# Kernel optimization log

Measured on AMD Instinct MI355X. Metric: run time of the kernel, lower is better.

## Reference

```python
import jax, jax.numpy as jnp
import numpy as np

VOCAB = 780
HIDDEN = 256
DEPTH = 6
N_NODES = 65536
N_MESS = 131072
MAX_NEI = 5
N_TREES = 2048


def setup_inputs() -> dict:
    key = jax.random.key(0)
    ks = jax.random.split(key, 16)
    s = 0.05  # weight scale to avoid gate saturation
    return {
        "fnode": jax.random.randint(ks[0], (N_NODES,), 0, VOCAB),
        "fmess": jax.random.randint(ks[1], (N_MESS,), 0, N_NODES),
        "node_graph": jax.random.randint(ks[2], (N_NODES, MAX_NEI), 0, N_MESS),
        "mess_graph": jax.random.randint(ks[3], (N_MESS, MAX_NEI), 0, N_MESS),
        "scope_ids": jnp.sort(jax.random.randint(ks[4], (N_NODES,), 0, N_TREES)),
        "emb": jax.random.normal(ks[5], (VOCAB, HIDDEN), jnp.float32) * s,
        "Wz_w": jax.random.normal(ks[6], (2 * HIDDEN, HIDDEN), jnp.float32) * s,
        "Wz_b": jax.random.normal(ks[7], (HIDDEN,), jnp.float32) * s,
        "Wr_w": jax.random.normal(ks[8], (HIDDEN, HIDDEN), jnp.float32) * s,
        "Ur_w": jax.random.normal(ks[9], (HIDDEN, HIDDEN), jnp.float32) * s,
        "Ur_b": jax.random.normal(ks[10], (HIDDEN,), jnp.float32) * s,
        "Wh_w": jax.random.normal(ks[11], (2 * HIDDEN, HIDDEN), jnp.float32) * s,
        "Wh_b": jax.random.normal(ks[12], (HIDDEN,), jnp.float32) * s,
        "out_w": jax.random.normal(ks[13], (2 * HIDDEN, HIDDEN), jnp.float32) * s,
        "out_b": jax.random.normal(ks[14], (HIDDEN,), jnp.float32) * s,
    }


def reference(fnode, fmess, node_graph, mess_graph, scope_ids,
              emb, Wz_w, Wz_b, Wr_w, Ur_w, Ur_b, Wh_w, Wh_b, out_w, out_b):
    x_node = emb[fnode]            # [N, H] embedding lookup
    x = x_node[fmess]              # [M, H] source-node feature per message
    M = mess_graph.shape[0]
    mask = jnp.ones((M, 1), x.dtype).at[0].set(0.0)  # message 0 is padding
    r1 = x @ Wr_w                  # W_r(x), constant across depth (no bias)

    def gru_step(h, _):
        h_nei = h[mess_graph]                                  # [M, K, H] gather
        sum_h = h_nei.sum(axis=1)                              # [M, H]
        z = jax.nn.sigmoid(jnp.concatenate([x, sum_h], 1) @ Wz_w + Wz_b)
        r = jax.nn.sigmoid(r1[:, None, :] + h_nei @ Ur_w + Ur_b)  # [M, K, H]
        sum_gh = (r * h_nei).sum(axis=1)
        pre_h = jnp.tanh(jnp.concatenate([x, sum_gh], 1) @ Wh_w + Wh_b)
        h_new = ((1.0 - z) * sum_h + z * pre_h) * mask
        return h_new, None

    h0 = jnp.zeros((M, HIDDEN), x.dtype)
    h, _ = jax.lax.scan(gru_step, h0, None, length=DEPTH)

    mess_nei = h[node_graph].sum(axis=1)                       # [N, H]
    node_vec = jax.nn.relu(jnp.concatenate([x_node, mess_nei], 1) @ out_w + out_b)

    # per-tree mean over contiguous scopes (segment mean)
    sums = jax.ops.segment_sum(node_vec, scope_ids, num_segments=N_TREES)
    counts = jax.ops.segment_sum(jnp.ones((node_vec.shape[0],), node_vec.dtype),
                                 scope_ids, num_segments=N_TREES)
    return sums / jnp.maximum(counts, 1.0)[:, None]
```

## Files before the change

kernel.cpp:

```cpp
#include <hip/hip_runtime.h>


#define HD 256
#define NNODES 65536
#define NMESS 131072
#define NVOCAB 780
#define NTREES 2048
#define MAXNEI 5
#define BMF 32
#define LDF 264
#define ROWB 768

typedef short bfrag __attribute__((ext_vector_type(8)));
typedef short s16x8 __attribute__((ext_vector_type(8)));
typedef float f32x4v __attribute__((ext_vector_type(4)));
typedef float f32x2 __attribute__((ext_vector_type(2)));
typedef unsigned int u32x4 __attribute__((ext_vector_type(4)));
typedef unsigned int u32x2 __attribute__((ext_vector_type(2)));
typedef unsigned short ush;
typedef unsigned char u8;

__device__ __forceinline__ float bf2f(ush u) {
    union { unsigned int u; float f; } v; v.u = ((unsigned int)u) << 16; return v.f;
}
__device__ __forceinline__ float bfu_lo(unsigned int w) {
    union { unsigned int u; float f; } v; v.u = w << 16; return v.f;
}
__device__ __forceinline__ float bfu_hi(unsigned int w) {
    union { unsigned int u; float f; } v; v.u = w & 0xffff0000u; return v.f;
}
__device__ __forceinline__ ush f2bf_fast(float f) {
    union { float f; unsigned int u; } v; v.f = f;
    return (ush)((v.u + 0x8000u) >> 16);
}
__device__ __forceinline__ unsigned int pack2bf(float hi, float lo) {
    union { float f; unsigned int u; } a, b; a.f = hi; b.f = lo;
    return __builtin_amdgcn_perm(a.u + 0x8000u, b.u + 0x8000u, 0x07060302u);
}
__device__ __forceinline__ float sigm(float x) {
    return __builtin_amdgcn_rcpf(1.f + __expf(-x));
}
__device__ __forceinline__ float tanh_fast(float x) {
    return 1.f - 2.f * __builtin_amdgcn_rcpf(__expf(2.f * x) + 1.f);
}
__device__ __forceinline__ u32x2 pack8fp8(const float* f) {
    int lo = __builtin_amdgcn_cvt_pk_fp8_f32(f[0], f[1], 0, 0);
    lo = __builtin_amdgcn_cvt_pk_fp8_f32(f[2], f[3], lo, 1);
    int hi = __builtin_amdgcn_cvt_pk_fp8_f32(f[4], f[5], 0, 0);
    hi = __builtin_amdgcn_cvt_pk_fp8_f32(f[6], f[7], hi, 1);
    u32x2 o; o.x = (unsigned int)lo; o.y = (unsigned int)hi; return o;
}
__device__ __forceinline__ void fp8x8_to_f32(u32x2 v, float* f) {
    f32x2 a = __builtin_amdgcn_cvt_pk_f32_fp8((int)v.x, false);
    f32x2 b = __builtin_amdgcn_cvt_pk_f32_fp8((int)v.x, true);
    f32x2 c = __builtin_amdgcn_cvt_pk_f32_fp8((int)v.y, false);
    f32x2 d = __builtin_amdgcn_cvt_pk_f32_fp8((int)v.y, true);
    f[0] = a.x; f[1] = a.y; f[2] = b.x; f[3] = b.y;
    f[4] = c.x; f[5] = c.y; f[6] = d.x; f[7] = d.y;
}

__global__ __launch_bounds__(256) void prep_tables_sk(
    const float* __restrict__ emb,
    const float* __restrict__ Wz_w, const float* __restrict__ Wz_b,
    const float* __restrict__ Wr_w, const float* __restrict__ Ur_b,
    const float* __restrict__ Wh_w, const float* __restrict__ Wh_b,
    const float* __restrict__ out_w, const float* __restrict__ out_b,
    float* __restrict__ embR, float* __restrict__ embZ,
    float* __restrict__ embH, float* __restrict__ embO)
{
    __shared__ __align__(16) float e[4][64];
    int t = threadIdx.x;
    int b0 = blockIdx.x * 4;
    int k0 = blockIdx.y * 64;
    e[t >> 6][t & 63] = emb[(b0 + (t >> 6)) * HD + k0 + (t & 63)];
    __syncthreads();
    float aR[4] = {0,0,0,0}, aZ[4] = {0,0,0,0}, aH[4] = {0,0,0,0}, aO[4] = {0,0,0,0};
    for (int kk = 0; kk < 64; kk++) {
        int k = k0 + kk;
        float wr = Wr_w[k * HD + t];
        float wz = Wz_w[k * HD + t];
        float wh = Wh_w[k * HD + t];
        float wo = out_w[k * HD + t];
        #pragma unroll
        for (int r = 0; r < 4; r++) {
            float ev = e[r][kk];
            aR[r] += ev * wr; aZ[r] += ev * wz; aH[r] += ev * wh; aO[r] += ev * wo;
        }
    }
    if (blockIdx.y == 0) {
        float br = Ur_b[t], bz = Wz_b[t], bh = Wh_b[t], bo = out_b[t];
        #pragma unroll
        for (int r = 0; r < 4; r++) { aR[r] += br; aZ[r] += bz; aH[r] += bh; aO[r] += bo; }
    }
    #pragma unroll
    for (int r = 0; r < 4; r++) {
        atomicAdd(&embR[(b0 + r) * HD + t], aR[r]);
        atomicAdd(&embZ[(b0 + r) * HD + t], aZ[r]);
        atomicAdd(&embH[(b0 + r) * HD + t], aH[r]);
        atomicAdd(&embO[(b0 + r) * HD + t], aO[r]);
    }
}

__global__ __launch_bounds__(256) void h1fill(
    const float* __restrict__ embZ, const float* __restrict__ embH,
    ush* __restrict__ h1tab)
{
    int i = blockIdx.x * HD + threadIdx.x;
    h1tab[i] = f2bf_fast(sigm(embZ[i]) * tanh_fast(embH[i]));
}

__global__ __launch_bounds__(256) void h1u_sk(
    const ush* __restrict__ h1tab, const float* __restrict__ Ur_w,
    float* __restrict__ embU)
{
    __shared__ __align__(16) float e[4][64];
    int t = threadIdx.x;
    int b0 = blockIdx.x * 4;
    int k0 = blockIdx.y * 64;
    e[t >> 6][t & 63] = bf2f(h1tab[(b0 + (t >> 6)) * HD + k0 + (t & 63)]);
    __syncthreads();
    float aU[4] = {0,0,0,0};
    for (int kk = 0; kk < 64; kk++) {
        float w = Ur_w[(k0 + kk) * HD + t];
        #pragma unroll
        for (int r = 0; r < 4; r++) aU[r] += e[r][kk] * w;
    }
    #pragma unroll
    for (int r = 0; r < 4; r++) atomicAdd(&embU[(b0 + r) * HD + t], aU[r]);
}

__global__ __launch_bounds__(256) void prep_wt(
    const float* __restrict__ Ur_w, const float* __restrict__ Wz_w,
    const float* __restrict__ Wh_w, const float* __restrict__ out_w,
    ush* __restrict__ Wo_p,
    ush* __restrict__ Wz_p, ush* __restrict__ Wh_p, ush* __restrict__ Ur_p)
{
    int idx = blockIdx.x * 256 + threadIdx.x;
    int n = idx >> 8, k = idx & 255;
    int paddr = ((((n >> 4) * 8 + (k >> 5)) * 64 + ((k >> 3) & 3) * 16 + (n & 15)) << 3) + (k & 7);
    Wo_p[paddr] = f2bf_fast(out_w[(HD + k) * HD + n]);
    Wz_p[paddr] = f2bf_fast(Wz_w[(HD + k) * HD + n]);
    Wh_p[paddr] = f2bf_fast(Wh_w[(HD + k) * HD + n]);
    Ur_p[paddr] = f2bf_fast(Ur_w[k * HD + n]);
}

__global__ __launch_bounds__(256) void prep_vmess(
    const int* __restrict__ fnode, const int* __restrict__ fmess,
    int* __restrict__ v_mess)
{
    int m = blockIdx.x * 256 + threadIdx.x;
    v_mess[m] = fnode[fmess[m]];
}

__global__ __launch_bounds__(256) void fill_h1(
    const ush* __restrict__ h1tab, const float* __restrict__ embU,
    const int* __restrict__ v_mess, u8* __restrict__ HM)
{
    int t = blockIdx.x * 256 + threadIdx.x;
    int m = t >> 5;
    int c = (t & 31) * 8;
    int v = v_mess[m];
    s16x8 o = *(const s16x8*)&h1tab[v * HD + c];
    float u[8];
    *(float4*)&u[0] = *(const float4*)&embU[v * HD + c];
    *(float4*)&u[4] = *(const float4*)&embU[v * HD + c + 4];
    u32x2 up = pack8fp8(u);
    if (m == 0) { o = (s16x8){0,0,0,0,0,0,0,0}; up.x = up.y = 0; }
    u8* row = HM + (size_t)m * ROWB;
    *(s16x8*)(row + 2 * c) = o;
    *(u32x2*)(row + 512 + c) = up;
}

template<int EMIT_HU>
__global__ __launch_bounds__(256, 4) void fused_step(
    const u8* __restrict__ HM, const int* __restrict__ mg,
    const int* __restrict__ v_mess,
    const float* __restrict__ embR, const float* __restrict__ embZ,
    const float* __restrict__ embH,
    const ush* __restrict__ Wz_p, const ush* __restrict__ Wh_p,
    const ush* __restrict__ Ur_p,
    u8* __restrict__ HM_next)
{
    __shared__ __align__(16) ush sh[BMF * LDF];
    __shared__ __align__(16) ush sg[BMF * LDF];
    int tid = threadIdx.x;
    int wv = tid >> 6, lane = tid & 63;
    int quad = lane >> 4, l16 = lane & 15;
    int m0 = blockIdx.x * BMF;

    #pragma unroll 2
    for (int it = 0; it < 4; it++) {
        int g = it * 256 + tid;
        int ml = g >> 5;
        int c = (g & 31) * 8;
        int m = m0 + ml;
        int v = v_mess[m];
        float rb[8];
        *(float4*)&rb[0] = *(const float4*)&embR[v * HD + c];
        *(float4*)&rb[4] = *(const float4*)&embR[v * HD + c + 4];
        float ah[8] = {0,0,0,0,0,0,0,0};
        float ag[8] = {0,0,0,0,0,0,0,0};
        #pragma unroll
        for (int kn = 0; kn < MAXNEI; kn++) {
            int j = mg[m * MAXNEI + kn];
            const u8* row = HM + (size_t)j * ROWB;
            s16x8 hv = *(const s16x8*)(row + 2 * c);
            u32x2 uv8 = *(const u32x2*)(row + 512 + c);
            float uf[8];
            fp8x8_to_f32(uv8, uf);
            #pragma unroll
            for (int e = 0; e < 8; e++) {
                float hf = bf2f((ush)hv[e]);
                ah[e] += hf;
                ag[e] += sigm(rb[e] + uf[e]) * hf;
            }
        }
        uint4 oh, og;
        oh.x = pack2bf(ah[1], ah[0]); oh.y = pack2bf(ah[3], ah[2]);
        oh.z = pack2bf(ah[5], ah[4]); oh.w = pack2bf(ah[7], ah[6]);
        og.x = pack2bf(ag[1], ag[0]); og.y = pack2bf(ag[3], ag[2]);
        og.z = pack2bf(ag[5], ag[4]); og.w = pack2bf(ag[7], ag[6]);
        *(uint4*)&sh[ml * LDF + c] = oh;
        *(uint4*)&sg[ml * LDF + c] = og;
    }
    __syncthreads();

    f32x4v az[2][4] = {}, ap[2][4] = {};
    #pragma unroll
    for (int ksi = 0; ksi < 8; ksi++) {
        int ks = ksi * 32;
        bfrag ahf[2], agf[2], bz[4], bh[4];
        #pragma unroll
        for (int i = 0; i < 2; i++) {
            ahf[i] = *(const bfrag*)&sh[(i * 16 + l16) * LDF + ks + quad * 8];
            agf[i] = *(const bfrag*)&sg[(i * 16 + l16) * LDF + ks + quad * 8];
        }
        #pragma unroll
        for (int j = 0; j < 4; j++) {
            int f = ((wv * 4 + j) * 8 + ksi) * 64 + lane;
            bz[j] = *(const bfrag*)&Wz_p[(size_t)f * 8];
            bh[j] = *(const bfrag*)&Wh_p[(size_t)f * 8];
        }
        #pragma unroll
        for (int i = 0; i < 2; i++)
            #pragma unroll
            for (int j = 0; j < 4; j++) {
                az[i][j] = __builtin_amdgcn_mfma_f32_16x16x32_bf16(ahf[i], bz[j], az[i][j], 0, 0, 0);
                ap[i][j] = __builtin_amdgcn_mfma_f32_16x16x32_bf16(agf[i], bh[j], ap[i][j], 0, 0, 0);
            }
    }

    #pragma unroll
    for (int i = 0; i < 2; i++) {
        #pragma unroll
        for (int r = 0; r < 4; r++) {
            int rl = i * 16 + quad * 4 + r;
            int Rg = m0 + rl;
            int v = v_mess[Rg];
            #pragma unroll
            for (int j = 0; j < 4; j++) {
                int col = wv * 64 + j * 16 + l16;
                float z = sigm(az[i][j][r] + embZ[v * HD + col]);
                float pre = tanh_fast(ap[i][j][r] + embH[v * HD + col]);
                float shv = bf2f(sh[rl * LDF + col]);
                float hn = (1.f - z) * shv + z * pre;
                if (Rg == 0) hn = 0.f;
                az[i][j][r] = hn;
            }
        }
    }
    __syncthreads();

    #pragma unroll
    for (int i = 0; i < 2; i++)
        #pragma unroll
        for (int j = 0; j < 4; j++) {
            int col = wv * 64 + j * 16 + l16;
            #pragma unroll
            for (int r = 0; r < 4; r++)
                sg[(i * 16 + quad * 4 + r) * LDF + col] = f2bf_fast(az[i][j][r]);
        }
    __syncthreads();
    #pragma unroll
    for (int it = 0; it < 4; it++) {
        int g = it * 256 + tid;
        int ml = g >> 5;
        int c = (g & 31) * 8;
        u32x4 w = *(const u32x4*)&sg[ml * LDF + c];
        __builtin_nontemporal_store(w, (u32x4*)(HM_next + (size_t)(m0 + ml) * ROWB + 2 * c));
    }

    if (EMIT_HU) {
        f32x4v au[2][4] = {};
        #pragma unroll
        for (int ksi = 0; ksi < 8; ksi++) {
            int ks = ksi * 32;
            bfrag af[2], bu[4];
            #pragma unroll
            for (int i = 0; i < 2; i++)
                af[i] = *(const bfrag*)&sg[(i * 16 + l16) * LDF + ks + quad * 8];
            #pragma unroll
            for (int j = 0; j < 4; j++) {
                int f = ((wv * 4 + j) * 8 + ksi) * 64 + lane;
                bu[j] = *(const bfrag*)&Ur_p[(size_t)f * 8];
            }
            #pragma unroll
            for (int i = 0; i < 2; i++)
                #pragma unroll
                for (int j = 0; j < 4; j++)
                    au[i][j] = __builtin_amdgcn_mfma_f32_16x16x32_bf16(af[i], bu[j], au[i][j], 0, 0, 0);
        }
        #pragma unroll
        for (int i = 0; i < 2; i++)
            #pragma unroll
            for (int j = 0; j < 4; j++) {
                int col = wv * 64 + j * 16 + l16;
                #pragma unroll
                for (int r = 0; r < 4; r++)
                    sh[(i * 16 + quad * 4 + r) * LDF + col] = f2bf_fast(au[i][j][r]);
            }
        __syncthreads();
        #pragma unroll
        for (int it = 0; it < 4; it++) {
            int g = it * 256 + tid;
            int ml = g >> 5;
            int c = (g & 31) * 8;
            uint4 w = *(const uint4*)&sh[ml * LDF + c];
            float f[8] = { bfu_lo(w.x), bfu_hi(w.x), bfu_lo(w.y), bfu_hi(w.y),
                           bfu_lo(w.z), bfu_hi(w.z), bfu_lo(w.w), bfu_hi(w.w) };
            u32x2 o = pack8fp8(f);
            __builtin_nontemporal_store(o, (u32x2*)(HM_next + (size_t)(m0 + ml) * ROWB + 512 + c));
        }
    }
}

__global__ __launch_bounds__(256) void gather_out(
    const u8* __restrict__ HM, const int* __restrict__ ng,
    const int* __restrict__ fnode, const float* __restrict__ embO,
    const ush* __restrict__ Wo_p, float* __restrict__ node_vec)
{
    __shared__ __align__(16) ush sh[BMF * LDF];
    int tid = threadIdx.x;
    int wv = tid >> 6, lane = tid & 63;
    int quad = lane >> 4, l16 = lane & 15;
    int n0 = blockIdx.x * BMF;

    #pragma unroll 2
    for (int it = 0; it < 4; it++) {
        int g = it * 256 + tid;
        int ml = g >> 5;
        int c = (g & 31) * 8;
        int n = n0 + ml;
        float a[8] = {0,0,0,0,0,0,0,0};
        #pragma unroll
        for (int kn = 0; kn < MAXNEI; kn++) {
            int j = ng[n * MAXNEI + kn];
            s16x8 hv = *(const s16x8*)(HM + (size_t)j * ROWB + 2 * c);
            #pragma unroll
            for (int e = 0; e < 8; e++) a[e] += bf2f((ush)hv[e]);
        }
        uint4 o;
        o.x = pack2bf(a[1], a[0]); o.y = pack2bf(a[3], a[2]);
        o.z = pack2bf(a[5], a[4]); o.w = pack2bf(a[7], a[6]);
        *(uint4*)&sh[ml * LDF + c] = o;
    }
    __syncthreads();

    f32x4v acc[2][4] = {};
    #pragma unroll
    for (int ksi = 0; ksi < 8; ksi++) {
        int ks = ksi * 32;
        bfrag af[2], bo[4];
        #pragma unroll
        for (int i = 0; i < 2; i++)
            af[i] = *(const bfrag*)&sh[(i * 16 + l16) * LDF + ks + quad * 8];
        #pragma unroll
        for (int j = 0; j < 4; j++) {
            int f = ((wv * 4 + j) * 8 + ksi) * 64 + lane;
            bo[j] = *(const bfrag*)&Wo_p[(size_t)f * 8];
        }
        #pragma unroll
        for (int i = 0; i < 2; i++)
            #pragma unroll
            for (int j = 0; j < 4; j++)
                acc[i][j] = __builtin_amdgcn_mfma_f32_16x16x32_bf16(af[i], bo[j], acc[i][j], 0, 0, 0);
    }

    #pragma unroll
    for (int i = 0; i < 2; i++) {
        #pragma unroll
        for (int r = 0; r < 4; r++) {
            int Rn = n0 + i * 16 + quad * 4 + r;
            int v = fnode[Rn];
            #pragma unroll
            for (int j = 0; j < 4; j++) {
                int col = wv * 64 + j * 16 + l16;
                float o = acc[i][j][r] + embO[v * HD + col];
                node_vec[(size_t)Rn * HD + col] = fmaxf(o, 0.f);
            }
        }
    }
}

__device__ __forceinline__ int lower_bound_dev(const int* a, int n, int key) {
    int lo = 0, hi = n;
    while (lo < hi) { int mid = (lo + hi) >> 1; if (a[mid] < key) lo = mid + 1; else hi = mid; }
    return lo;
}

__global__ __launch_bounds__(256) void segment_mean(
    const float* __restrict__ node_vec, const int* __restrict__ scope,
    float* __restrict__ out)
{
    int t = blockIdx.x;
    int c = threadIdx.x;
    int lo = lower_bound_dev(scope, NNODES, t);
    int hi = lower_bound_dev(scope, NNODES, t + 1);
    float acc = 0.f;
    for (int n = lo; n < hi; n++) acc += node_vec[(size_t)n * HD + c];
    int cnt = hi - lo;
    out[t * HD + c] = cnt > 0 ? acc / (float)cnt : 0.f;
}

extern "C" void kernel_launch(void* const* d_in, const int* in_sizes, int n_in,
                              void* d_out, int out_size, void* d_ws, size_t ws_size,
                              hipStream_t stream)
{
    const int*   fnode      = (const int*)d_in[0];
    const int*   fmess      = (const int*)d_in[1];
    const int*   node_graph = (const int*)d_in[2];
    const int*   mess_graph = (const int*)d_in[3];
    const int*   scope_ids  = (const int*)d_in[4];
    const float* emb        = (const float*)d_in[5];
    const float* Wz_w       = (const float*)d_in[6];
    const float* Wz_b       = (const float*)d_in[7];
    const float* Wr_w       = (const float*)d_in[8];
    const float* Ur_w       = (const float*)d_in[9];
    const float* Ur_b       = (const float*)d_in[10];
    const float* Wh_w       = (const float*)d_in[11];
    const float* Wh_b       = (const float*)d_in[12];
    const float* out_w      = (const float*)d_in[13];
    const float* out_b      = (const float*)d_in[14];

    char* ws = (char*)d_ws;
    const size_t HMB = (size_t)NMESS * ROWB;
    u8* HM0 = (u8*)ws; ws += HMB;
    u8* HM1 = (u8*)ws; ws += HMB;
    float* embR = (float*)ws; ws += (size_t)NVOCAB * HD * 4;
    float* embZ = (float*)ws; ws += (size_t)NVOCAB * HD * 4;
    float* embH = (float*)ws; ws += (size_t)NVOCAB * HD * 4;
    float* embO = (float*)ws; ws += (size_t)NVOCAB * HD * 4;
    float* embU = (float*)ws; ws += (size_t)NVOCAB * HD * 4;
    ush* h1tab = (ush*)ws; ws += (size_t)NVOCAB * HD * 2;
    ush* Wo_p  = (ush*)ws; ws += (size_t)HD * HD * 2;
    ush* Wz_p  = (ush*)ws; ws += (size_t)HD * HD * 2;
    ush* Wh_p  = (ush*)ws; ws += (size_t)HD * HD * 2;
    ush* Ur_p  = (ush*)ws; ws += (size_t)HD * HD * 2;
    int* v_mess = (int*)ws; ws += (size_t)NMESS * 4;
    if ((size_t)(ws - (char*)d_ws) > ws_size) return;

    hipMemsetAsync(embR, 0, (size_t)5 * NVOCAB * HD * 4, stream);
    prep_tables_sk<<<dim3(NVOCAB / 4, 4), 256, 0, stream>>>(
        emb, Wz_w, Wz_b, Wr_w, Ur_b, Wh_w, Wh_b, out_w, out_b,
        embR, embZ, embH, embO);
    h1fill<<<NVOCAB, 256, 0, stream>>>(embZ, embH, h1tab);
    h1u_sk<<<dim3(NVOCAB / 4, 4), 256, 0, stream>>>(h1tab, Ur_w, embU);
    prep_wt<<<HD * HD / 256, 256, 0, stream>>>(Ur_w, Wz_w, Wh_w, out_w,
                                               Wo_p, Wz_p, Wh_p, Ur_p);
    prep_vmess<<<NMESS / 256, 256, 0, stream>>>(fnode, fmess, v_mess);
    fill_h1<<<NMESS * 32 / 256, 256, 0, stream>>>(h1tab, embU, v_mess, HM0);

    u8* hc = HM0; u8* hn = HM1;
    for (int d = 1; d < 5; d++) {
        fused_step<1><<<NMESS / BMF, 256, 0, stream>>>(hc, mess_graph, v_mess,
                                                       embR, embZ, embH,
                                                       Wz_p, Wh_p, Ur_p, hn);
        u8* t = hc; hc = hn; hn = t;
    }
    fused_step<0><<<NMESS / BMF, 256, 0, stream>>>(hc, mess_graph, v_mess,
                                                   embR, embZ, embH,
                                                   Wz_p, Wh_p, Ur_p, hn);
    hc = hn;

    float* node_vec = (float*)(hc == HM0 ? HM1 : HM0);
    gather_out<<<NNODES / BMF, 256, 0, stream>>>(hc, node_graph, fnode, embO,
                                                 Wo_p, node_vec);
    segment_mean<<<NTREES, 256, 0, stream>>>(node_vec, scope_ids, (float*)d_out);
}
```

Baseline: 1.062 ms.

## Swizzle LDS tiles, hoist neighbor index loads, raise occupancy, drop nontemporal stores

Replaces the padded shared-memory row stride with an XOR-swizzled 16-byte-chunk layout, which shrinks LDS per block while trying to keep MFMA operand reads free of bank conflicts. The five neighbor indices are loaded up front so the gather loads can be issued back to back. The launch bound's minimum blocks per multiprocessor goes from 4 to 5, and the output stores become ordinary cached stores instead of nontemporal ones. Tighter register limits at the higher occupancy could cause spills, and the scalar epilogue LDS accesses through the swizzle may hit some bank conflicts.

Measured after the change: 1.714 ms. 1.61x slower.

```diff
diff --git a/kernel.cpp b/kernel.cpp
--- a/kernel.cpp
+++ b/kernel.cpp
@@ -8,14 +8,14 @@
 #define NTREES 2048
 #define MAXNEI 5
 #define BMF 32
-#define LDF 264
 #define ROWB 768
+
+#define SWZ16(row, chunk) ((row) * 256 + ((((chunk) ^ ((row) & 7))) << 3))
 
 typedef short bfrag __attribute__((ext_vector_type(8)));
 typedef short s16x8 __attribute__((ext_vector_type(8)));
 typedef float f32x4v __attribute__((ext_vector_type(4)));
 typedef float f32x2 __attribute__((ext_vector_type(2)));
-typedef unsigned int u32x4 __attribute__((ext_vector_type(4)));
 typedef unsigned int u32x2 __attribute__((ext_vector_type(2)));
 typedef unsigned short ush;
 typedef unsigned char u8;
@@ -172,7 +172,7 @@
 }
 
 template<int EMIT_HU>
-__global__ __launch_bounds__(256, 4) void fused_step(
+__global__ __launch_bounds__(256, 5) void fused_step(
     const u8* __restrict__ HM, const int* __restrict__ mg,
     const int* __restrict__ v_mess,
     const float* __restrict__ embR, const float* __restrict__ embZ,
@@ -181,8 +181,8 @@
     const ush* __restrict__ Ur_p,
     u8* __restrict__ HM_next)
 {
-    __shared__ __align__(16) ush sh[BMF * LDF];
-    __shared__ __align__(16) ush sg[BMF * LDF];
+    __shared__ __align__(16) ush sh[BMF * 256];
+    __shared__ __align__(16) ush sg[BMF * 256];
     int tid = threadIdx.x;
     int wv = tid >> 6, lane = tid & 63;
     int quad = lane >> 4, l16 = lane & 15;
@@ -192,9 +192,13 @@
     for (int it = 0; it < 4; it++) {
         int g = it * 256 + tid;
         int ml = g >> 5;
-        int c = (g & 31) * 8;
+        int ch = g & 31;
+        int c = ch * 8;
         int m = m0 + ml;
         int v = v_mess[m];
+        int jj[MAXNEI];
+        #pragma unroll
+        for (int kn = 0; kn < MAXNEI; kn++) jj[kn] = mg[m * MAXNEI + kn];
         float rb[8];
         *(float4*)&rb[0] = *(const float4*)&embR[v * HD + c];
         *(float4*)&rb[4] = *(const float4*)&embR[v * HD + c + 4];
@@ -202,8 +206,7 @@
         float ag[8] = {0,0,0,0,0,0,0,0};
         #pragma unroll
         for (int kn = 0; kn < MAXNEI; kn++) {
-            int j = mg[m * MAXNEI + kn];
-            const u8* row = HM + (size_t)j * ROWB;
+            const u8* row = HM + (size_t)jj[kn] * ROWB;
             s16x8 hv = *(const s16x8*)(row + 2 * c);
             u32x2 uv8 = *(const u32x2*)(row + 512 + c);
             float uf[8];
@@ -220,20 +223,21 @@
         oh.z = pack2bf(ah[5], ah[4]); oh.w = pack2bf(ah[7], ah[6]);
         og.x = pack2bf(ag[1], ag[0]); og.y = pack2bf(ag[3], ag[2]);
         og.z = pack2bf(ag[5], ag[4]); og.w = pack2bf(ag[7], ag[6]);
-        *(uint4*)&sh[ml * LDF + c] = oh;
-        *(uint4*)&sg[ml * LDF + c] = og;
+        *(uint4*)&sh[SWZ16(ml, ch)] = oh;
+        *(uint4*)&sg[SWZ16(ml, ch)] = og;
     }
     __syncthreads();
 
     f32x4v az[2][4] = {}, ap[2][4] = {};
     #pragma unroll
     for (int ksi = 0; ksi < 8; ksi++) {
-        int ks = ksi * 32;
         bfrag ahf[2], agf[2], bz[4], bh[4];
         #pragma unroll
         for (int i = 0; i < 2; i++) {
-            ahf[i] = *(const bfrag*)&sh[(i * 16 + l16) * LDF + ks + quad * 8];
-            agf[i] = *(const bfrag*)&sg[(i * 16 + l16) * LDF + ks + quad * 8];
+            int rr = i * 16 + l16;
+            int q = ksi * 4 + quad;
+            ahf[i] = *(const bfrag*)&sh[SWZ16(rr, q)];
+            agf[i] = *(const bfrag*)&sg[SWZ16(rr, q)];
         }
         #pragma unroll
         for (int j = 0; j < 4; j++) {
@@ -262,7 +266,7 @@
                 int col = wv * 64 + j * 16 + l16;
                 float z = sigm(az[i][j][r] + embZ[v * HD + col]);
                 float pre = tanh_fast(ap[i][j][r] + embH[v * HD + col]);
-                float shv = bf2f(sh[rl * LDF + col]);
+                float shv = bf2f(sh[SWZ16(rl, col >> 3) + (col & 7)]);
                 float hn = (1.f - z) * shv + z * pre;
                 if (Rg == 0) hn = 0.f;
                 az[i][j][r] = hn;
@@ -277,28 +281,32 @@
         for (int j = 0; j < 4; j++) {
             int col = wv * 64 + j * 16 + l16;
             #pragma unroll
-            for (int r = 0; r < 4; r++)
-                sg[(i * 16 + quad * 4 + r) * LDF + col] = f2bf_fast(az[i][j][r]);
+            for (int r = 0; r < 4; r++) {
+                int rl = i * 16 + quad * 4 + r;
+                sg[SWZ16(rl, col >> 3) + (col & 7)] = f2bf_fast(az[i][j][r]);
+            }
         }
     __syncthreads();
     #pragma unroll
     for (int it = 0; it < 4; it++) {
         int g = it * 256 + tid;
         int ml = g >> 5;
-        int c = (g & 31) * 8;
-        u32x4 w = *(const u32x4*)&sg[ml * LDF + c];
-        __builtin_nontemporal_store(w, (u32x4*)(HM_next + (size_t)(m0 + ml) * ROWB + 2 * c));
+        int ch = g & 31;
+        *(uint4*)(HM_next + (size_t)(m0 + ml) * ROWB + ch * 16) =
+            *(const uint4*)&sg[SWZ16(ml, ch)];
     }
 
     if (EMIT_HU) {
         f32x4v au[2][4] = {};
         #pragma unroll
         for (int ksi = 0; ksi < 8; ksi++) {
-            int ks = ksi * 32;
             bfrag af[2], bu[4];
             #pragma unroll
-            for (int i = 0; i < 2; i++)
-                af[i] = *(const bfrag*)&sg[(i * 16 + l16) * LDF + ks + quad * 8];
+            for (int i = 0; i < 2; i++) {
+                int rr = i * 16 + l16;
+                int q = ksi * 4 + quad;
+                af[i] = *(const bfrag*)&sg[SWZ16(rr, q)];
+            }
             #pragma unroll
             for (int j = 0; j < 4; j++) {
                 int f = ((wv * 4 + j) * 8 + ksi) * 64 + lane;
@@ -316,20 +324,22 @@
             for (int j = 0; j < 4; j++) {
                 int col = wv * 64 + j * 16 + l16;
                 #pragma unroll
-                for (int r = 0; r < 4; r++)
-                    sh[(i * 16 + quad * 4 + r) * LDF + col] = f2bf_fast(au[i][j][r]);
+                for (int r = 0; r < 4; r++) {
+                    int rl = i * 16 + quad * 4 + r;
+                    sh[SWZ16(rl, col >> 3) + (col & 7)] = f2bf_fast(au[i][j][r]);
+                }
             }
         __syncthreads();
         #pragma unroll
         for (int it = 0; it < 4; it++) {
             int g = it * 256 + tid;
             int ml = g >> 5;
-            int c = (g & 31) * 8;
-            uint4 w = *(const uint4*)&sh[ml * LDF + c];
+            int ch = g & 31;
+            uint4 w = *(const uint4*)&sh[SWZ16(ml, ch)];
             float f[8] = { bfu_lo(w.x), bfu_hi(w.x), bfu_lo(w.y), bfu_hi(w.y),
                            bfu_lo(w.z), bfu_hi(w.z), bfu_lo(w.w), bfu_hi(w.w) };
             u32x2 o = pack8fp8(f);
-            __builtin_nontemporal_store(o, (u32x2*)(HM_next + (size_t)(m0 + ml) * ROWB + 512 + c));
+            *(u32x2*)(HM_next + (size_t)(m0 + ml) * ROWB + 512 + ch * 8) = o;
         }
     }
 }
@@ -339,7 +349,7 @@
     const int* __restrict__ fnode, const float* __restrict__ embO,
     const ush* __restrict__ Wo_p, float* __restrict__ node_vec)
 {
-    __shared__ __align__(16) ush sh[BMF * LDF];
+    __shared__ __align__(16) ush sh[BMF * 256];
     int tid = threadIdx.x;
     int wv = tid >> 6, lane = tid & 63;
     int quad = lane >> 4, l16 = lane & 15;
@@ -349,7 +359,8 @@
     for (int it = 0; it < 4; it++) {
         int g = it * 256 + tid;
         int ml = g >> 5;
-        int c = (g & 31) * 8;
+        int ch = g & 31;
+        int c = ch * 8;
         int n = n0 + ml;
         float a[8] = {0,0,0,0,0,0,0,0};
         #pragma unroll
@@ -362,18 +373,20 @@
         uint4 o;
         o.x = pack2bf(a[1], a[0]); o.y = pack2bf(a[3], a[2]);
         o.z = pack2bf(a[5], a[4]); o.w = pack2bf(a[7], a[6]);
-        *(uint4*)&sh[ml * LDF + c] = o;
+        *(uint4*)&sh[SWZ16(ml, ch)] = o;
     }
     __syncthreads();
 
     f32x4v acc[2][4] = {};
     #pragma unroll
     for (int ksi = 0; ksi < 8; ksi++) {
-        int ks = ksi * 32;
         bfrag af[2], bo[4];
         #pragma unroll
-        for (int i = 0; i < 2; i++)
-            af[i] = *(const bfrag*)&sh[(i * 16 + l16) * LDF + ks + quad * 8];
+        for (int i = 0; i < 2; i++) {
+            int rr = i * 16 + l16;
+            int q = ksi * 4 + quad;
+            af[i] = *(const bfrag*)&sh[SWZ16(rr, q)];
+        }
         #pragma unroll
         for (int j = 0; j < 4; j++) {
             int f = ((wv * 4 + j) * 8 + ksi) * 64 + lane;
```

## Fuse initial message fill into first GRU step via vocab-table gathers

Applied to the files above, without the earlier changes.

Removes the kernel that materialised the depth-1 message state for every message and instead has the first fused step gather neighbor state directly from small per-vocab tables through v_mess, masking the padding message. An fp8 copy of the Ur projection table is packed once for this path. This avoids writing and rereading a large per-message buffer, at the cost of an extra indirect index load per neighbor. Nontemporal stores of the next state are also replaced with ordinary stores.

Measured after the change: 1.035 ms. -2.5%, faster.

```diff
diff --git a/kernel.cpp b/kernel.cpp
--- a/kernel.cpp
+++ b/kernel.cpp
@@ -15,7 +15,6 @@
 typedef short s16x8 __attribute__((ext_vector_type(8)));
 typedef float f32x4v __attribute__((ext_vector_type(4)));
 typedef float f32x2 __attribute__((ext_vector_type(2)));
-typedef unsigned int u32x4 __attribute__((ext_vector_type(4)));
 typedef unsigned int u32x2 __attribute__((ext_vector_type(2)));
 typedef unsigned short ush;
 typedef unsigned char u8;
@@ -129,6 +128,18 @@
     for (int r = 0; r < 4; r++) atomicAdd(&embU[(b0 + r) * HD + t], aU[r]);
 }
 
+__global__ __launch_bounds__(256) void u8pack(
+    const float* __restrict__ embU, u8* __restrict__ embU8)
+{
+    int t = blockIdx.x * 256 + threadIdx.x;
+    if (t >= NVOCAB * HD / 8) return;
+    float u[8];
+    *(float4*)&u[0] = *(const float4*)&embU[t * 8];
+    *(float4*)&u[4] = *(const float4*)&embU[t * 8 + 4];
+    u32x2 o = pack8fp8(u);
+    *(u32x2*)&embU8[t * 8] = o;
+}
+
 __global__ __launch_bounds__(256) void prep_wt(
     const float* __restrict__ Ur_w, const float* __restrict__ Wz_w,
     const float* __restrict__ Wh_w, const float* __restrict__ out_w,
@@ -152,29 +163,11 @@
     v_mess[m] = fnode[fmess[m]];
 }
 
-__global__ __launch_bounds__(256) void fill_h1(
-    const ush* __restrict__ h1tab, const float* __restrict__ embU,
-    const int* __restrict__ v_mess, u8* __restrict__ HM)
-{
-    int t = blockIdx.x * 256 + threadIdx.x;
-    int m = t >> 5;
-    int c = (t & 31) * 8;
-    int v = v_mess[m];
-    s16x8 o = *(const s16x8*)&h1tab[v * HD + c];
-    float u[8];
-    *(float4*)&u[0] = *(const float4*)&embU[v * HD + c];
-    *(float4*)&u[4] = *(const float4*)&embU[v * HD + c + 4];
-    u32x2 up = pack8fp8(u);
-    if (m == 0) { o = (s16x8){0,0,0,0,0,0,0,0}; up.x = up.y = 0; }
-    u8* row = HM + (size_t)m * ROWB;
-    *(s16x8*)(row + 2 * c) = o;
-    *(u32x2*)(row + 512 + c) = up;
-}
-
-template<int EMIT_HU>
+template<int EMIT_HU, int TAB>
 __global__ __launch_bounds__(256, 4) void fused_step(
     const u8* __restrict__ HM, const int* __restrict__ mg,
     const int* __restrict__ v_mess,
+    const ush* __restrict__ h1tab, const u8* __restrict__ embU8,
     const float* __restrict__ embR, const float* __restrict__ embZ,
     const float* __restrict__ embH,
     const ush* __restrict__ Wz_p, const ush* __restrict__ Wh_p,
@@ -203,14 +196,25 @@
         #pragma unroll
         for (int kn = 0; kn < MAXNEI; kn++) {
             int j = mg[m * MAXNEI + kn];
-            const u8* row = HM + (size_t)j * ROWB;
-            s16x8 hv = *(const s16x8*)(row + 2 * c);
-            u32x2 uv8 = *(const u32x2*)(row + 512 + c);
+            s16x8 hv;
+            u32x2 uv8;
+            float msk;
+            if (TAB) {
+                int vmj = v_mess[j];
+                hv = *(const s16x8*)&h1tab[vmj * HD + c];
+                uv8 = *(const u32x2*)&embU8[vmj * HD + c];
+                msk = (j != 0) ? 1.f : 0.f;
+            } else {
+                const u8* row = HM + (size_t)j * ROWB;
+                hv = *(const s16x8*)(row + 2 * c);
+                uv8 = *(const u32x2*)(row + 512 + c);
+                msk = 1.f;
+            }
             float uf[8];
             fp8x8_to_f32(uv8, uf);
             #pragma unroll
             for (int e = 0; e < 8; e++) {
-                float hf = bf2f((ush)hv[e]);
+                float hf = bf2f((ush)hv[e]) * msk;
                 ah[e] += hf;
                 ag[e] += sigm(rb[e] + uf[e]) * hf;
             }
@@ -286,8 +290,8 @@
         int g = it * 256 + tid;
         int ml = g >> 5;
         int c = (g & 31) * 8;
-        u32x4 w = *(const u32x4*)&sg[ml * LDF + c];
-        __builtin_nontemporal_store(w, (u32x4*)(HM_next + (size_t)(m0 + ml) * ROWB + 2 * c));
+        *(uint4*)(HM_next + (size_t)(m0 + ml) * ROWB + 2 * c) =
+            *(const uint4*)&sg[ml * LDF + c];
     }
 
     if (EMIT_HU) {
@@ -329,7 +333,7 @@
             float f[8] = { bfu_lo(w.x), bfu_hi(w.x), bfu_lo(w.y), bfu_hi(w.y),
                            bfu_lo(w.z), bfu_hi(w.z), bfu_lo(w.w), bfu_hi(w.w) };
             u32x2 o = pack8fp8(f);
-            __builtin_nontemporal_store(o, (u32x2*)(HM_next + (size_t)(m0 + ml) * ROWB + 512 + c));
+            *(u32x2*)(HM_next + (size_t)(m0 + ml) * ROWB + 512 + c) = o;
         }
     }
 }
@@ -452,6 +456,7 @@
     float* embO = (float*)ws; ws += (size_t)NVOCAB * HD * 4;
     float* embU = (float*)ws; ws += (size_t)NVOCAB * HD * 4;
     ush* h1tab = (ush*)ws; ws += (size_t)NVOCAB * HD * 2;
+    u8* embU8  = (u8*)ws;  ws += (size_t)NVOCAB * HD;
     ush* Wo_p  = (ush*)ws; ws += (size_t)HD * HD * 2;
     ush* Wz_p  = (ush*)ws; ws += (size_t)HD * HD * 2;
     ush* Wh_p  = (ush*)ws; ws += (size_t)HD * HD * 2;
@@ -465,21 +470,24 @@
         embR, embZ, embH, embO);
     h1fill<<<NVOCAB, 256, 0, stream>>>(embZ, embH, h1tab);
     h1u_sk<<<dim3(NVOCAB / 4, 4), 256, 0, stream>>>(h1tab, Ur_w, embU);
+    u8pack<<<(NVOCAB * HD / 8 + 255) / 256, 256, 0, stream>>>(embU, embU8);
     prep_wt<<<HD * HD / 256, 256, 0, stream>>>(Ur_w, Wz_w, Wh_w, out_w,
                                                Wo_p, Wz_p, Wh_p, Ur_p);
     prep_vmess<<<NMESS / 256, 256, 0, stream>>>(fnode, fmess, v_mess);
-    fill_h1<<<NMESS * 32 / 256, 256, 0, stream>>>(h1tab, embU, v_mess, HM0);
-
+
+    fused_step<1, 1><<<NMESS / BMF, 256, 0, stream>>>(
+        nullptr, mess_graph, v_mess, h1tab, embU8,
+        embR, embZ, embH, Wz_p, Wh_p, Ur_p, HM0);
     u8* hc = HM0; u8* hn = HM1;
-    for (int d = 1; d < 5; d++) {
-        fused_step<1><<<NMESS / BMF, 256, 0, stream>>>(hc, mess_graph, v_mess,
-                                                       embR, embZ, embH,
-                                                       Wz_p, Wh_p, Ur_p, hn);
+    for (int d = 2; d < 5; d++) {
+        fused_step<1, 0><<<NMESS / BMF, 256, 0, stream>>>(
+            hc, mess_graph, v_mess, nullptr, nullptr,
+            embR, embZ, embH, Wz_p, Wh_p, Ur_p, hn);
         u8* t = hc; hc = hn; hn = t;
     }
-    fused_step<0><<<NMESS / BMF, 256, 0, stream>>>(hc, mess_graph, v_mess,
-                                                   embR, embZ, embH,
-                                                   Wz_p, Wh_p, Ur_p, hn);
+    fused_step<0, 0><<<NMESS / BMF, 256, 0, stream>>>(
+        hc, mess_graph, v_mess, nullptr, nullptr,
+        embR, embZ, embH, Wz_p, Wh_p, Ur_p, hn);
     hc = hn;
 
     float* node_vec = (float*)(hc == HM0 ? HM1 : HM0);
```
